# Optimization experiments

Measured on AMD Instinct MI355X. Metric: run time of the kernel, lower is better.

The kernel has to match this reference:

```python
import jax, jax.numpy as jnp
import numpy as np

H, B, I = 1024, 64, 128
W_SCALE = 0.192
BETA = 10.0 / W_SCALE   # softplus-like sharpness 'b' in source
DT = 0.1
DELTA_T = 1.0
Z_MIN, Z_MAX = 0.001, 0.1


def setup_inputs() -> dict:
    key = jax.random.key(0)
    ks = jax.random.split(key, 12)
    s = 1.0 / np.sqrt(H)  # nn.init.uniform_(param, -1/sqrt(H), 1/sqrt(H))
    u = lambda k, shp: jax.random.uniform(k, shp, jnp.float32, -s, s)
    return {
        "x": jax.random.normal(ks[0], (I, B), jnp.float32),
        "v_t": jnp.zeros((B, H), jnp.float32),
        "X": jnp.ones((B, H, H), jnp.float32),            # depression state x=1
        "U": jnp.full((B, H, H), 0.9, jnp.float32),       # facilitation state U=0.9
        "raw_w_r": u(ks[1], (H, H)),
        "p_r": u(ks[2], (H, I)),
        "b_r": u(ks[3], (H, 1)),
        "g_z": u(ks[4], (H, 1)),
        "c_x": u(ks[5], (H, H)),
        "c_u": u(ks[6], (H, H)),
        "c_U": u(ks[7], (H, H)),
        "a_exc": jax.random.uniform(ks[8], (), jnp.float32, -s, s),
        "a_inh": jax.random.uniform(ks[9], (), jnp.float32, -s, s),
    }


def reference(x, v_t, X, U, raw_w_r, p_r, b_r, g_z, c_x, c_u, c_U, a_exc, a_inh):
    sig = jax.nn.sigmoid
    # rectified recurrent weights: (1/b) * log(cosh(b * raw)) -- same formula in
    # all four quadrants of the source, so apply it to the whole matrix.
    w_r = jnp.log(jnp.cosh(BETA * raw_w_r)) / BETA          # (H, H), >= 0
    w_z = jnp.abs(w_r)
    p_z = jnp.abs(p_r)
    # Dale gain: excitatory gain for first half of rows, inhibitory for second.
    a = jnp.concatenate([jnp.full((H // 2, 1), 1.0) * a_exc,
                         jnp.full((H // 2, 1), 1.0) * a_inh], axis=0)
    A = 10.0 * sig(a)                                        # (H, 1)

    vt = v_t.T                                               # (H, B)
    r = sig(vt)                                              # (H, B) firing rates
    rb = r.T[:, :, None]                                     # (B, H, 1) -> r_t[j,b]

    # synaptic depression X: X' = z_x + (1-z_x)X - dt * U * X * r_pre
    z_x = Z_MIN + (Z_MAX - Z_MIN) * sig(c_x)                 # (H, H)
    X_new = z_x + (1.0 - z_x) * X - DELTA_T * U * (X * rb)   # (B, H, H)

    # synaptic facilitation U: U' = Ucap*z_u + (1-z_u)U + dt * Ucap * (1-U) * r_pre
    z_u = Z_MIN + (Z_MAX - Z_MIN) * sig(c_u)
    Ucap = 0.9 * sig(c_U)                                    # (H, H)
    U_new = Ucap * z_u + (1.0 - z_u) * U + DELTA_T * Ucap * ((1.0 - U) * rb)
    U_new = jnp.clip(U_new, jax.lax.stop_gradient(Ucap)[None], 1.0)

    # gate z_t = dt * sigmoid(w_z (A*r) + p_z x + g_z)
    z_t = DT * sig(w_z @ (A * r) + p_z @ x + g_z)            # (H, B)

    # membrane update: per-batch effective weights (X*U*w_r) applied to rates
    rec = jnp.einsum('bjk,kb->jb', X_new * U_new * w_r, r)   # (H, B)
    v_new = (1.0 - z_t) * vt + DT * (rec + p_r @ x + b_r)    # (H, B)
    v_new = v_new.T                                          # (B, H)

    return v_new
```

## Files before the change

### kernel.cpp

```cpp
#include <hip/hip_runtime.h>
#include <cstddef>

#define Hdim 1024
#define Bdim 64
#define Idim 128

#define BETA_F 52.083333333333336f
#define INV_BETA_F 0.0192f
#define LN2_F 0.6931471805599453f

__device__ __forceinline__ float sigf(float x) {
    return 1.0f / (1.0f + __expf(-x));
}

__device__ __forceinline__ float logcoshf_(float t) {
    float a = fabsf(t);
    return a + log1pf(__expf(-2.0f * a)) - LN2_F;
}

__global__ void pre_kernel(const float* __restrict__ x,
                           const float* __restrict__ v_t,
                           const float* __restrict__ p_r,
                           const float* __restrict__ b_r,
                           const float* __restrict__ g_z,
                           float* __restrict__ r_ws,
                           float* __restrict__ membx,
                           float* __restrict__ gatex) {
    const int j = blockIdx.x;
    const int b = threadIdx.x;
    const float* pr = p_r + (size_t)j * Idim;
    float accm = 0.0f, accg = 0.0f;
#pragma unroll 4
    for (int i = 0; i < Idim; ++i) {
        float p  = pr[i];
        float xv = x[i * Bdim + b];
        accm = fmaf(p, xv, accm);
        accg = fmaf(fabsf(p), xv, accg);
    }
    membx[j * Bdim + b] = accm + b_r[j];
    gatex[j * Bdim + b] = accg + g_z[j];

    int id = j * Bdim + b;
    r_ws[id] = sigf(v_t[id]);
}

__global__ __launch_bounds__(256, 4) void main_kernel(
    const float* __restrict__ X,
    const float* __restrict__ U,
    const float* __restrict__ raw_w_r,
    const float* __restrict__ c_x,
    const float* __restrict__ c_u,
    const float* __restrict__ c_U,
    const float* __restrict__ v_t,
    const float* __restrict__ a_exc,
    const float* __restrict__ a_inh,
    const float* __restrict__ r_ws,
    const float* __restrict__ membx,
    const float* __restrict__ gatex,
    float* __restrict__ out) {
    __shared__ __align__(16) float s_zx[Hdim];
    __shared__ __align__(16) float s_zu[Hdim];
    __shared__ __align__(16) float s_uc[Hdim];
    __shared__ __align__(16) float s_wr[Hdim];
    __shared__ __align__(16) float s_wa[Hdim];

    const int j   = blockIdx.x;
    const int tid = threadIdx.x;

    const float Aexc = 10.0f * sigf(a_exc[0]);
    const float Ainh = 10.0f * sigf(a_inh[0]);

    {
        const int k = tid * 4;
        const size_t ro = (size_t)j * Hdim + k;
        float4 rw = *(const float4*)(raw_w_r + ro);
        float4 cx = *(const float4*)(c_x + ro);
        float4 cu = *(const float4*)(c_u + ro);
        float4 cN = *(const float4*)(c_U + ro);
        const float A = (k < Hdim / 2) ? Aexc : Ainh;

        float w0 = logcoshf_(BETA_F * rw.x) * INV_BETA_F;
        float w1 = logcoshf_(BETA_F * rw.y) * INV_BETA_F;
        float w2 = logcoshf_(BETA_F * rw.z) * INV_BETA_F;
        float w3 = logcoshf_(BETA_F * rw.w) * INV_BETA_F;
        s_wr[k + 0] = w0; s_wa[k + 0] = w0 * A;
        s_wr[k + 1] = w1; s_wa[k + 1] = w1 * A;
        s_wr[k + 2] = w2; s_wa[k + 2] = w2 * A;
        s_wr[k + 3] = w3; s_wa[k + 3] = w3 * A;

        s_zx[k + 0] = 0.001f + 0.099f * sigf(cx.x);
        s_zx[k + 1] = 0.001f + 0.099f * sigf(cx.y);
        s_zx[k + 2] = 0.001f + 0.099f * sigf(cx.z);
        s_zx[k + 3] = 0.001f + 0.099f * sigf(cx.w);

        s_zu[k + 0] = 0.001f + 0.099f * sigf(cu.x);
        s_zu[k + 1] = 0.001f + 0.099f * sigf(cu.y);
        s_zu[k + 2] = 0.001f + 0.099f * sigf(cu.z);
        s_zu[k + 3] = 0.001f + 0.099f * sigf(cu.w);

        s_uc[k + 0] = 0.9f * sigf(cN.x);
        s_uc[k + 1] = 0.9f * sigf(cN.y);
        s_uc[k + 2] = 0.9f * sigf(cN.z);
        s_uc[k + 3] = 0.9f * sigf(cN.w);
    }
    __syncthreads();

    const int wave = tid >> 6;
    const int lane = tid & 63;

    for (int b = wave; b < Bdim; b += 4) {
        const float* Xb = X + (size_t)b * Hdim * Hdim + (size_t)j * Hdim;
        const float* Ub = U + (size_t)b * Hdim * Hdim + (size_t)j * Hdim;
        const float* rb = r_ws + b * Hdim;
        const float rj = rb[j];

        float rec = 0.0f, gate = 0.0f;
#pragma unroll
        for (int it = 0; it < 4; ++it) {
            const int k = (it * 64 + lane) * 4;
            float4 Xv = *(const float4*)(Xb + k);
            float4 Uv = *(const float4*)(Ub + k);
            float4 rv = *(const float4*)(rb + k);
            float4 zx = *(const float4*)(s_zx + k);
            float4 zu = *(const float4*)(s_zu + k);
            float4 uc = *(const float4*)(s_uc + k);
            float4 wr = *(const float4*)(s_wr + k);
            float4 wa = *(const float4*)(s_wa + k);

#define COMPONENT(c)                                                          \
    {                                                                         \
        float xn = zx.c + (1.0f - zx.c) * Xv.c - Uv.c * Xv.c * rj;            \
        float un = uc.c * zu.c + (1.0f - zu.c) * Uv.c +                       \
                   uc.c * (1.0f - Uv.c) * rj;                                 \
        un = fminf(fmaxf(un, uc.c), 1.0f);                                    \
        rec  = fmaf(xn * un * wr.c, rv.c, rec);                               \
        gate = fmaf(wa.c, rv.c, gate);                                        \
    }
            COMPONENT(x)
            COMPONENT(y)
            COMPONENT(z)
            COMPONENT(w)
#undef COMPONENT
        }

#pragma unroll
        for (int off = 32; off > 0; off >>= 1) {
            rec  += __shfl_xor(rec, off, 64);
            gate += __shfl_xor(gate, off, 64);
        }

        if (lane == 0) {
            float z  = 0.1f * sigf(gate + gatex[j * Bdim + b]);
            float vt = v_t[(size_t)b * Hdim + j];
            float vn = (1.0f - z) * vt + 0.1f * (rec + membx[j * Bdim + b]);
            out[(size_t)b * Hdim + j] = vn;
        }
    }
}

extern "C" void kernel_launch(void* const* d_in, const int* in_sizes, int n_in,
                              void* d_out, int out_size, void* d_ws, size_t ws_size,
                              hipStream_t stream) {
    const float* x       = (const float*)d_in[0];
    const float* v_t     = (const float*)d_in[1];
    const float* X       = (const float*)d_in[2];
    const float* U       = (const float*)d_in[3];
    const float* raw_w_r = (const float*)d_in[4];
    const float* p_r     = (const float*)d_in[5];
    const float* b_r     = (const float*)d_in[6];
    const float* g_z     = (const float*)d_in[7];
    const float* c_x     = (const float*)d_in[8];
    const float* c_u     = (const float*)d_in[9];
    const float* c_U     = (const float*)d_in[10];
    const float* a_exc   = (const float*)d_in[11];
    const float* a_inh   = (const float*)d_in[12];

    float* out = (float*)d_out;

    float* r_ws  = (float*)d_ws;
    float* membx = r_ws + Bdim * Hdim;
    float* gatex = membx + Hdim * Bdim;

    pre_kernel<<<dim3(Hdim), dim3(Bdim), 0, stream>>>(
        x, v_t, p_r, b_r, g_z, r_ws, membx, gatex);

    main_kernel<<<dim3(Hdim), dim3(256), 0, stream>>>(
        X, U, raw_w_r, c_x, c_u, c_U, v_t, a_exc, a_inh,
        r_ws, membx, gatex, out);
}
```

Before: 550.8 us.

## Split batch across grid y and batch 4 rows per wave for memory parallelism

The main kernel grid becomes 1024x4, with each wave handling 4 batch entries at once. Loads for X, U and r are issued for all 4 entries before the arithmetic, which raises memory-level parallelism on the bandwidth-bound stream over the 2x256MB X/U tensors. The A-weighted shared array is dropped; the gate is accumulated as separate excitatory and inhibitory partial sums and scaled by A at the end. In exchange, each of the 4 blocks per row recomputes the per-row logcosh and sigmoid tables, and register pressure rises.

```diff
diff --git a/kernel.cpp b/kernel.cpp
--- a/kernel.cpp
+++ b/kernel.cpp
@@ -62,13 +62,9 @@
     __shared__ __align__(16) float s_zu[Hdim];
     __shared__ __align__(16) float s_uc[Hdim];
     __shared__ __align__(16) float s_wr[Hdim];
-    __shared__ __align__(16) float s_wa[Hdim];
 
     const int j   = blockIdx.x;
     const int tid = threadIdx.x;
-
-    const float Aexc = 10.0f * sigf(a_exc[0]);
-    const float Ainh = 10.0f * sigf(a_inh[0]);
 
     {
         const int k = tid * 4;
@@ -77,16 +73,11 @@
         float4 cx = *(const float4*)(c_x + ro);
         float4 cu = *(const float4*)(c_u + ro);
         float4 cN = *(const float4*)(c_U + ro);
-        const float A = (k < Hdim / 2) ? Aexc : Ainh;
-
-        float w0 = logcoshf_(BETA_F * rw.x) * INV_BETA_F;
-        float w1 = logcoshf_(BETA_F * rw.y) * INV_BETA_F;
-        float w2 = logcoshf_(BETA_F * rw.z) * INV_BETA_F;
-        float w3 = logcoshf_(BETA_F * rw.w) * INV_BETA_F;
-        s_wr[k + 0] = w0; s_wa[k + 0] = w0 * A;
-        s_wr[k + 1] = w1; s_wa[k + 1] = w1 * A;
-        s_wr[k + 2] = w2; s_wa[k + 2] = w2 * A;
-        s_wr[k + 3] = w3; s_wa[k + 3] = w3 * A;
+
+        s_wr[k + 0] = logcoshf_(BETA_F * rw.x) * INV_BETA_F;
+        s_wr[k + 1] = logcoshf_(BETA_F * rw.y) * INV_BETA_F;
+        s_wr[k + 2] = logcoshf_(BETA_F * rw.z) * INV_BETA_F;
+        s_wr[k + 3] = logcoshf_(BETA_F * rw.w) * INV_BETA_F;
 
         s_zx[k + 0] = 0.001f + 0.099f * sigf(cx.x);
         s_zx[k + 1] = 0.001f + 0.099f * sigf(cx.y);
@@ -107,52 +98,85 @@
 
     const int wave = tid >> 6;
     const int lane = tid & 63;
-
-    for (int b = wave; b < Bdim; b += 4) {
-        const float* Xb = X + (size_t)b * Hdim * Hdim + (size_t)j * Hdim;
-        const float* Ub = U + (size_t)b * Hdim * Hdim + (size_t)j * Hdim;
-        const float* rb = r_ws + b * Hdim;
-        const float rj = rb[j];
-
-        float rec = 0.0f, gate = 0.0f;
-#pragma unroll
-        for (int it = 0; it < 4; ++it) {
-            const int k = (it * 64 + lane) * 4;
-            float4 Xv = *(const float4*)(Xb + k);
-            float4 Uv = *(const float4*)(Ub + k);
-            float4 rv = *(const float4*)(rb + k);
-            float4 zx = *(const float4*)(s_zx + k);
-            float4 zu = *(const float4*)(s_zu + k);
-            float4 uc = *(const float4*)(s_uc + k);
-            float4 wr = *(const float4*)(s_wr + k);
-            float4 wa = *(const float4*)(s_wa + k);
-
+    const int b0   = blockIdx.y * 16 + wave * 4;
+
+    const float* Xr[4];
+    const float* Ur[4];
+    const float* rr[4];
+    float rj[4];
+#pragma unroll
+    for (int bb = 0; bb < 4; ++bb) {
+        const int b = b0 + bb;
+        Xr[bb] = X + ((size_t)b * Hdim + j) * Hdim;
+        Ur[bb] = U + ((size_t)b * Hdim + j) * Hdim;
+        rr[bb] = r_ws + b * Hdim;
+        rj[bb] = rr[bb][j];
+    }
+
+    float rec[4] = {0.f, 0.f, 0.f, 0.f};
+    float ge[4]  = {0.f, 0.f, 0.f, 0.f};
+    float gi[4]  = {0.f, 0.f, 0.f, 0.f};
+
+#pragma unroll
+    for (int chunk = 0; chunk < 4; ++chunk) {
+        const int k = (chunk * 64 + lane) * 4;
+        float4 zx = *(const float4*)(s_zx + k);
+        float4 zu = *(const float4*)(s_zu + k);
+        float4 uc = *(const float4*)(s_uc + k);
+        float4 wr = *(const float4*)(s_wr + k);
+
+        float4 Xv[4], Uv[4], rv[4];
+#pragma unroll
+        for (int bb = 0; bb < 4; ++bb) {
+            Xv[bb] = *(const float4*)(Xr[bb] + k);
+            Uv[bb] = *(const float4*)(Ur[bb] + k);
+            rv[bb] = *(const float4*)(rr[bb] + k);
+        }
+
+#pragma unroll
+        for (int bb = 0; bb < 4; ++bb) {
+            float g = 0.0f;
 #define COMPONENT(c)                                                          \
     {                                                                         \
-        float xn = zx.c + (1.0f - zx.c) * Xv.c - Uv.c * Xv.c * rj;            \
-        float un = uc.c * zu.c + (1.0f - zu.c) * Uv.c +                       \
-                   uc.c * (1.0f - Uv.c) * rj;                                 \
+        float xn = zx.c + (1.0f - zx.c) * Xv[bb].c - Uv[bb].c * Xv[bb].c * rj[bb]; \
+        float un = uc.c * zu.c + (1.0f - zu.c) * Uv[bb].c +                   \
+                   uc.c * (1.0f - Uv[bb].c) * rj[bb];                         \
         un = fminf(fmaxf(un, uc.c), 1.0f);                                    \
-        rec  = fmaf(xn * un * wr.c, rv.c, rec);                               \
-        gate = fmaf(wa.c, rv.c, gate);                                        \
+        rec[bb] = fmaf(xn * un * wr.c, rv[bb].c, rec[bb]);                    \
+        g       = fmaf(wr.c, rv[bb].c, g);                                    \
     }
             COMPONENT(x)
             COMPONENT(y)
             COMPONENT(z)
             COMPONENT(w)
 #undef COMPONENT
-        }
-
-#pragma unroll
-        for (int off = 32; off > 0; off >>= 1) {
-            rec  += __shfl_xor(rec, off, 64);
-            gate += __shfl_xor(gate, off, 64);
-        }
-
-        if (lane == 0) {
-            float z  = 0.1f * sigf(gate + gatex[j * Bdim + b]);
+            if (chunk < 2) ge[bb] += g; else gi[bb] += g;
+        }
+    }
+
+    const float Aexc = 10.0f * sigf(a_exc[0]);
+    const float Ainh = 10.0f * sigf(a_inh[0]);
+    float gate[4];
+#pragma unroll
+    for (int bb = 0; bb < 4; ++bb)
+        gate[bb] = fmaf(Aexc, ge[bb], Ainh * gi[bb]);
+
+#pragma unroll
+    for (int off = 32; off > 0; off >>= 1) {
+#pragma unroll
+        for (int bb = 0; bb < 4; ++bb) {
+            rec[bb]  += __shfl_xor(rec[bb], off, 64);
+            gate[bb] += __shfl_xor(gate[bb], off, 64);
+        }
+    }
+
+    if (lane == 0) {
+#pragma unroll
+        for (int bb = 0; bb < 4; ++bb) {
+            const int b = b0 + bb;
+            float z  = 0.1f * sigf(gate[bb] + gatex[j * Bdim + b]);
             float vt = v_t[(size_t)b * Hdim + j];
-            float vn = (1.0f - z) * vt + 0.1f * (rec + membx[j * Bdim + b]);
+            float vn = (1.0f - z) * vt + 0.1f * (rec[bb] + membx[j * Bdim + b]);
             out[(size_t)b * Hdim + j] = vn;
         }
     }
@@ -184,7 +208,7 @@
     pre_kernel<<<dim3(Hdim), dim3(Bdim), 0, stream>>>(
         x, v_t, p_r, b_r, g_z, r_ws, membx, gatex);
 
-    main_kernel<<<dim3(Hdim), dim3(256), 0, stream>>>(
+    main_kernel<<<dim3(Hdim, 4), dim3(256), 0, stream>>>(
         X, U, raw_w_r, c_x, c_u, c_U, v_t, a_exc, a_inh,
         r_ws, membx, gatex, out);
 }
```

Result: slower. 568.7 us (+3.2%).

## Precompute transformed weights and process two batches per wave

Applied to the files above, without the earlier changes.

Moves the logcosh and sigmoid transforms of the H×H parameter matrices into a separate elementwise kernel whose outputs go to workspace. The main kernel now gives each wave one row j and two batch entries, reusing the loaded parameter vectors across both batches. The gate computation applies the Dale gain after the reduction instead of storing a scaled copy of the weights. This adds a kernel launch and extra workspace traffic for four H×H arrays, and keeps a fallback path that recomputes the transforms inline when the workspace is too small. The dominant cost is still streaming the large X and U tensors.

```diff
diff --git a/kernel.cpp b/kernel.cpp
--- a/kernel.cpp
+++ b/kernel.cpp
@@ -44,13 +44,51 @@
     r_ws[id] = sigf(v_t[id]);
 }
 
-__global__ __launch_bounds__(256, 4) void main_kernel(
-    const float* __restrict__ X,
-    const float* __restrict__ U,
+__global__ __launch_bounds__(256) void transform_kernel(
     const float* __restrict__ raw_w_r,
     const float* __restrict__ c_x,
     const float* __restrict__ c_u,
     const float* __restrict__ c_U,
+    float* __restrict__ t_wr,
+    float* __restrict__ t_zx,
+    float* __restrict__ t_zu,
+    float* __restrict__ t_uc) {
+    const int i = (blockIdx.x * 256 + threadIdx.x) * 4;
+    float4 rw = *(const float4*)(raw_w_r + i);
+    float4 cx = *(const float4*)(c_x + i);
+    float4 cu = *(const float4*)(c_u + i);
+    float4 cN = *(const float4*)(c_U + i);
+    float4 o;
+    o.x = logcoshf_(BETA_F * rw.x) * INV_BETA_F;
+    o.y = logcoshf_(BETA_F * rw.y) * INV_BETA_F;
+    o.z = logcoshf_(BETA_F * rw.z) * INV_BETA_F;
+    o.w = logcoshf_(BETA_F * rw.w) * INV_BETA_F;
+    *(float4*)(t_wr + i) = o;
+    o.x = 0.001f + 0.099f * sigf(cx.x);
+    o.y = 0.001f + 0.099f * sigf(cx.y);
+    o.z = 0.001f + 0.099f * sigf(cx.z);
+    o.w = 0.001f + 0.099f * sigf(cx.w);
+    *(float4*)(t_zx + i) = o;
+    o.x = 0.001f + 0.099f * sigf(cu.x);
+    o.y = 0.001f + 0.099f * sigf(cu.y);
+    o.z = 0.001f + 0.099f * sigf(cu.z);
+    o.w = 0.001f + 0.099f * sigf(cu.w);
+    *(float4*)(t_zu + i) = o;
+    o.x = 0.9f * sigf(cN.x);
+    o.y = 0.9f * sigf(cN.y);
+    o.z = 0.9f * sigf(cN.z);
+    o.w = 0.9f * sigf(cN.w);
+    *(float4*)(t_uc + i) = o;
+}
+
+template <bool PRECOMP>
+__global__ __launch_bounds__(256, 8) void main_kernel(
+    const float* __restrict__ X,
+    const float* __restrict__ U,
+    const float* __restrict__ pw_,
+    const float* __restrict__ pzx_,
+    const float* __restrict__ pzu_,
+    const float* __restrict__ puc_,
     const float* __restrict__ v_t,
     const float* __restrict__ a_exc,
     const float* __restrict__ a_inh,
@@ -58,102 +96,120 @@
     const float* __restrict__ membx,
     const float* __restrict__ gatex,
     float* __restrict__ out) {
-    __shared__ __align__(16) float s_zx[Hdim];
-    __shared__ __align__(16) float s_zu[Hdim];
-    __shared__ __align__(16) float s_uc[Hdim];
-    __shared__ __align__(16) float s_wr[Hdim];
-    __shared__ __align__(16) float s_wa[Hdim];
-
-    const int j   = blockIdx.x;
-    const int tid = threadIdx.x;
+    const int wave = threadIdx.x >> 6;
+    const int lane = threadIdx.x & 63;
+    const int j    = blockIdx.y * 4 + wave;
+    const int b0   = blockIdx.x * 2;
+
+    const size_t prow = (size_t)j * Hdim;
+    const float* pw  = pw_  + prow;
+    const float* pzx = pzx_ + prow;
+    const float* pzu = pzu_ + prow;
+    const float* puc = puc_ + prow;
+
+    const float* X0 = X + ((size_t)b0 * Hdim + j) * Hdim;
+    const float* X1 = X0 + (size_t)Hdim * Hdim;
+    const float* U0 = U + ((size_t)b0 * Hdim + j) * Hdim;
+    const float* U1 = U0 + (size_t)Hdim * Hdim;
+    const float* rr0 = r_ws + b0 * Hdim;
+    const float* rr1 = rr0 + Hdim;
+
+    const float rj0 = rr0[j];
+    const float rj1 = rr1[j];
+
+    float rec0 = 0.f, rec1 = 0.f;
+    float ge0 = 0.f, ge1 = 0.f;
+    float gi0 = 0.f, gi1 = 0.f;
+
+#pragma unroll
+    for (int chunk = 0; chunk < 4; ++chunk) {
+        const int k = (chunk * 64 + lane) * 4;
+        float4 wr, zx, zu, uc;
+        if (PRECOMP) {
+            wr = *(const float4*)(pw + k);
+            zx = *(const float4*)(pzx + k);
+            zu = *(const float4*)(pzu + k);
+            uc = *(const float4*)(puc + k);
+        } else {
+            float4 rw = *(const float4*)(pw + k);
+            float4 cx = *(const float4*)(pzx + k);
+            float4 cu = *(const float4*)(pzu + k);
+            float4 cN = *(const float4*)(puc + k);
+            wr.x = logcoshf_(BETA_F * rw.x) * INV_BETA_F;
+            wr.y = logcoshf_(BETA_F * rw.y) * INV_BETA_F;
+            wr.z = logcoshf_(BETA_F * rw.z) * INV_BETA_F;
+            wr.w = logcoshf_(BETA_F * rw.w) * INV_BETA_F;
+            zx.x = 0.001f + 0.099f * sigf(cx.x);
+            zx.y = 0.001f + 0.099f * sigf(cx.y);
+            zx.z = 0.001f + 0.099f * sigf(cx.z);
+            zx.w = 0.001f + 0.099f * sigf(cx.w);
+            zu.x = 0.001f + 0.099f * sigf(cu.x);
+            zu.y = 0.001f + 0.099f * sigf(cu.y);
+            zu.z = 0.001f + 0.099f * sigf(cu.z);
+            zu.w = 0.001f + 0.099f * sigf(cu.w);
+            uc.x = 0.9f * sigf(cN.x);
+            uc.y = 0.9f * sigf(cN.y);
+            uc.z = 0.9f * sigf(cN.z);
+            uc.w = 0.9f * sigf(cN.w);
+        }
+        float4 r0 = *(const float4*)(rr0 + k);
+        float4 r1 = *(const float4*)(rr1 + k);
+        float4 Xv0 = *(const float4*)(X0 + k);
+        float4 Uv0 = *(const float4*)(U0 + k);
+        float4 Xv1 = *(const float4*)(X1 + k);
+        float4 Uv1 = *(const float4*)(U1 + k);
+
+        float g0 = 0.f, g1 = 0.f;
+#define COMPONENT(c)                                                          \
+    {                                                                         \
+        float xn0 = zx.c + (1.0f - zx.c) * Xv0.c - Uv0.c * Xv0.c * rj0;       \
+        float un0 = uc.c * zu.c + (1.0f - zu.c) * Uv0.c +                     \
+                    uc.c * (1.0f - Uv0.c) * rj0;                              \
+        un0 = fminf(fmaxf(un0, uc.c), 1.0f);                                  \
+        rec0 = fmaf(xn0 * un0 * wr.c, r0.c, rec0);                            \
+        g0   = fmaf(wr.c, r0.c, g0);                                          \
+        float xn1 = zx.c + (1.0f - zx.c) * Xv1.c - Uv1.c * Xv1.c * rj1;       \
+        float un1 = uc.c * zu.c + (1.0f - zu.c) * Uv1.c +                     \
+                    uc.c * (1.0f - Uv1.c) * rj1;                              \
+        un1 = fminf(fmaxf(un1, uc.c), 1.0f);                                  \
+        rec1 = fmaf(xn1 * un1 * wr.c, r1.c, rec1);                            \
+        g1   = fmaf(wr.c, r1.c, g1);                                          \
+    }
+        COMPONENT(x)
+        COMPONENT(y)
+        COMPONENT(z)
+        COMPONENT(w)
+#undef COMPONENT
+        if (chunk < 2) { ge0 += g0; ge1 += g1; }
+        else           { gi0 += g0; gi1 += g1; }
+    }
 
     const float Aexc = 10.0f * sigf(a_exc[0]);
     const float Ainh = 10.0f * sigf(a_inh[0]);
-
-    {
-        const int k = tid * 4;
-        const size_t ro = (size_t)j * Hdim + k;
-        float4 rw = *(const float4*)(raw_w_r + ro);
-        float4 cx = *(const float4*)(c_x + ro);
-        float4 cu = *(const float4*)(c_u + ro);
-        float4 cN = *(const float4*)(c_U + ro);
-        const float A = (k < Hdim / 2) ? Aexc : Ainh;
-
-        float w0 = logcoshf_(BETA_F * rw.x) * INV_BETA_F;
-        float w1 = logcoshf_(BETA_F * rw.y) * INV_BETA_F;
-        float w2 = logcoshf_(BETA_F * rw.z) * INV_BETA_F;
-        float w3 = logcoshf_(BETA_F * rw.w) * INV_BETA_F;
-        s_wr[k + 0] = w0; s_wa[k + 0] = w0 * A;
-        s_wr[k + 1] = w1; s_wa[k + 1] = w1 * A;
-        s_wr[k + 2] = w2; s_wa[k + 2] = w2 * A;
-        s_wr[k + 3] = w3; s_wa[k + 3] = w3 * A;
-
-        s_zx[k + 0] = 0.001f + 0.099f * sigf(cx.x);
-        s_zx[k + 1] = 0.001f + 0.099f * sigf(cx.y);
-        s_zx[k + 2] = 0.001f + 0.099f * sigf(cx.z);
-        s_zx[k + 3] = 0.001f + 0.099f * sigf(cx.w);
-
-        s_zu[k + 0] = 0.001f + 0.099f * sigf(cu.x);
-        s_zu[k + 1] = 0.001f + 0.099f * sigf(cu.y);
-        s_zu[k + 2] = 0.001f + 0.099f * sigf(cu.z);
-        s_zu[k + 3] = 0.001f + 0.099f * sigf(cu.w);
-
-        s_uc[k + 0] = 0.9f * sigf(cN.x);
-        s_uc[k + 1] = 0.9f * sigf(cN.y);
-        s_uc[k + 2] = 0.9f * sigf(cN.z);
-        s_uc[k + 3] = 0.9f * sigf(cN.w);
-    }
-    __syncthreads();
-
-    const int wave = tid >> 6;
-    const int lane = tid & 63;
-
-    for (int b = wave; b < Bdim; b += 4) {
-        const float* Xb = X + (size_t)b * Hdim * Hdim + (size_t)j * Hdim;
-        const float* Ub = U + (size_t)b * Hdim * Hdim + (size_t)j * Hdim;
-        const float* rb = r_ws + b * Hdim;
-        const float rj = rb[j];
-
-        float rec = 0.0f, gate = 0.0f;
+    float gate0 = fmaf(Aexc, ge0, Ainh * gi0);
+    float gate1 = fmaf(Aexc, ge1, Ainh * gi1);
+
 #pragma unroll
-        for (int it = 0; it < 4; ++it) {
-            const int k = (it * 64 + lane) * 4;
-            float4 Xv = *(const float4*)(Xb + k);
-            float4 Uv = *(const float4*)(Ub + k);
-            float4 rv = *(const float4*)(rb + k);
-            float4 zx = *(const float4*)(s_zx + k);
-            float4 zu = *(const float4*)(s_zu + k);
-            float4 uc = *(const float4*)(s_uc + k);
-            float4 wr = *(const float4*)(s_wr + k);
-            float4 wa = *(const float4*)(s_wa + k);
-
-#define COMPONENT(c)                                                          \
-    {                                                                         \
-        float xn = zx.c + (1.0f - zx.c) * Xv.c - Uv.c * Xv.c * rj;            \
-        float un = uc.c * zu.c + (1.0f - zu.c) * Uv.c +                       \
-                   uc.c * (1.0f - Uv.c) * rj;                                 \
-        un = fminf(fmaxf(un, uc.c), 1.0f);                                    \
-        rec  = fmaf(xn * un * wr.c, rv.c, rec);                               \
-        gate = fmaf(wa.c, rv.c, gate);                                        \
-    }
-            COMPONENT(x)
-            COMPONENT(y)
-            COMPONENT(z)
-            COMPONENT(w)
-#undef COMPONENT
+    for (int off = 32; off > 0; off >>= 1) {
+        rec0  += __shfl_xor(rec0, off, 64);
+        rec1  += __shfl_xor(rec1, off, 64);
+        gate0 += __shfl_xor(gate0, off, 64);
+        gate1 += __shfl_xor(gate1, off, 64);
+    }
+
+    if (lane == 0) {
+        {
+            float z  = 0.1f * sigf(gate0 + gatex[j * Bdim + b0]);
+            float vt = v_t[(size_t)b0 * Hdim + j];
+            out[(size_t)b0 * Hdim + j] =
+                (1.0f - z) * vt + 0.1f * (rec0 + membx[j * Bdim + b0]);
         }
-
-#pragma unroll
-        for (int off = 32; off > 0; off >>= 1) {
-            rec  += __shfl_xor(rec, off, 64);
-            gate += __shfl_xor(gate, off, 64);
-        }
-
-        if (lane == 0) {
-            float z  = 0.1f * sigf(gate + gatex[j * Bdim + b]);
+        {
+            const int b = b0 + 1;
+            float z  = 0.1f * sigf(gate1 + gatex[j * Bdim + b]);
             float vt = v_t[(size_t)b * Hdim + j];
-            float vn = (1.0f - z) * vt + 0.1f * (rec + membx[j * Bdim + b]);
-            out[(size_t)b * Hdim + j] = vn;
+            out[(size_t)b * Hdim + j] =
+                (1.0f - z) * vt + 0.1f * (rec1 + membx[j * Bdim + b]);
         }
     }
 }
@@ -180,11 +236,26 @@
     float* r_ws  = (float*)d_ws;
     float* membx = r_ws + Bdim * Hdim;
     float* gatex = membx + Hdim * Bdim;
+    float* t_wr  = gatex + Hdim * Bdim;
+    float* t_zx  = t_wr + (size_t)Hdim * Hdim;
+    float* t_zu  = t_zx + (size_t)Hdim * Hdim;
+    float* t_uc  = t_zu + (size_t)Hdim * Hdim;
+
+    const size_t needed =
+        (size_t)(3 * Bdim * Hdim + 4 * Hdim * Hdim) * sizeof(float);
 
     pre_kernel<<<dim3(Hdim), dim3(Bdim), 0, stream>>>(
         x, v_t, p_r, b_r, g_z, r_ws, membx, gatex);
 
-    main_kernel<<<dim3(Hdim), dim3(256), 0, stream>>>(
-        X, U, raw_w_r, c_x, c_u, c_U, v_t, a_exc, a_inh,
-        r_ws, membx, gatex, out);
-}
+    if (ws_size >= needed) {
+        transform_kernel<<<dim3(Hdim * Hdim / (256 * 4)), dim3(256), 0, stream>>>(
+            raw_w_r, c_x, c_u, c_U, t_wr, t_zx, t_zu, t_uc);
+        main_kernel<true><<<dim3(Bdim / 2, Hdim / 4), dim3(256), 0, stream>>>(
+            X, U, t_wr, t_zx, t_zu, t_uc, v_t, a_exc, a_inh,
+            r_ws, membx, gatex, out);
+    } else {
+        main_kernel<false><<<dim3(Bdim / 2, Hdim / 4), dim3(256), 0, stream>>>(
+            X, U, raw_w_r, c_x, c_u, c_U, v_t, a_exc, a_inh,
+            r_ws, membx, gatex, out);
+    }
+}
```

New measurement: 596.7 us. +8.3%, slower.

## Split batch across 2D grid and hoist all X/U loads for two batches

Applied to the files above, without the earlier changes.

The main kernel grid becomes (H, 2), so each block handles 32 batches and each wave handles 8, processed two at a time. All sixteen float4 X/U loads for the batch pair are issued up front to raise memory-level parallelism. The shared s_wa array is dropped and the Dale gain is applied after accumulating separate excitatory and inhibitory partial sums. The cost is doubled per-block prologue work (logcosh and sigmoid tables recomputed by twice as many blocks) and higher register pressure.

```diff
diff --git a/kernel.cpp b/kernel.cpp
--- a/kernel.cpp
+++ b/kernel.cpp
@@ -62,13 +62,9 @@
     __shared__ __align__(16) float s_zu[Hdim];
     __shared__ __align__(16) float s_uc[Hdim];
     __shared__ __align__(16) float s_wr[Hdim];
-    __shared__ __align__(16) float s_wa[Hdim];
 
     const int j   = blockIdx.x;
     const int tid = threadIdx.x;
-
-    const float Aexc = 10.0f * sigf(a_exc[0]);
-    const float Ainh = 10.0f * sigf(a_inh[0]);
 
     {
         const int k = tid * 4;
@@ -77,16 +73,11 @@
         float4 cx = *(const float4*)(c_x + ro);
         float4 cu = *(const float4*)(c_u + ro);
         float4 cN = *(const float4*)(c_U + ro);
-        const float A = (k < Hdim / 2) ? Aexc : Ainh;
-
-        float w0 = logcoshf_(BETA_F * rw.x) * INV_BETA_F;
-        float w1 = logcoshf_(BETA_F * rw.y) * INV_BETA_F;
-        float w2 = logcoshf_(BETA_F * rw.z) * INV_BETA_F;
-        float w3 = logcoshf_(BETA_F * rw.w) * INV_BETA_F;
-        s_wr[k + 0] = w0; s_wa[k + 0] = w0 * A;
-        s_wr[k + 1] = w1; s_wa[k + 1] = w1 * A;
-        s_wr[k + 2] = w2; s_wa[k + 2] = w2 * A;
-        s_wr[k + 3] = w3; s_wa[k + 3] = w3 * A;
+
+        s_wr[k + 0] = logcoshf_(BETA_F * rw.x) * INV_BETA_F;
+        s_wr[k + 1] = logcoshf_(BETA_F * rw.y) * INV_BETA_F;
+        s_wr[k + 2] = logcoshf_(BETA_F * rw.z) * INV_BETA_F;
+        s_wr[k + 3] = logcoshf_(BETA_F * rw.w) * INV_BETA_F;
 
         s_zx[k + 0] = 0.001f + 0.099f * sigf(cx.x);
         s_zx[k + 1] = 0.001f + 0.099f * sigf(cx.y);
@@ -107,53 +98,114 @@
 
     const int wave = tid >> 6;
     const int lane = tid & 63;
-
-    for (int b = wave; b < Bdim; b += 4) {
-        const float* Xb = X + (size_t)b * Hdim * Hdim + (size_t)j * Hdim;
-        const float* Ub = U + (size_t)b * Hdim * Hdim + (size_t)j * Hdim;
-        const float* rb = r_ws + b * Hdim;
-        const float rj = rb[j];
-
-        float rec = 0.0f, gate = 0.0f;
-#pragma unroll
-        for (int it = 0; it < 4; ++it) {
-            const int k = (it * 64 + lane) * 4;
-            float4 Xv = *(const float4*)(Xb + k);
-            float4 Uv = *(const float4*)(Ub + k);
-            float4 rv = *(const float4*)(rb + k);
-            float4 zx = *(const float4*)(s_zx + k);
-            float4 zu = *(const float4*)(s_zu + k);
-            float4 uc = *(const float4*)(s_uc + k);
-            float4 wr = *(const float4*)(s_wr + k);
-            float4 wa = *(const float4*)(s_wa + k);
-
-#define COMPONENT(c)                                                          \
+    const int base = blockIdx.y * 32 + wave * 8;
+
+    const float Aexc = 10.0f * sigf(a_exc[0]);
+    const float Ainh = 10.0f * sigf(a_inh[0]);
+
+    for (int it = 0; it < 4; ++it) {
+        const int b0 = base + 2 * it;
+        const float* X0 = X + ((size_t)b0 * Hdim + j) * Hdim;
+        const float* X1 = X0 + (size_t)Hdim * Hdim;
+        const float* U0 = U + ((size_t)b0 * Hdim + j) * Hdim;
+        const float* U1 = U0 + (size_t)Hdim * Hdim;
+        const float* rr0 = r_ws + b0 * Hdim;
+        const float* rr1 = rr0 + Hdim;
+
+        float4 xa0, xa1, xa2, xa3, ua0, ua1, ua2, ua3;
+        float4 xb0, xb1, xb2, xb3, ub0, ub1, ub2, ub3;
+        {
+            const int k0 = lane * 4;
+            xa0 = *(const float4*)(X0 + k0 + 0);
+            xa1 = *(const float4*)(X0 + k0 + 256);
+            xa2 = *(const float4*)(X0 + k0 + 512);
+            xa3 = *(const float4*)(X0 + k0 + 768);
+            ua0 = *(const float4*)(U0 + k0 + 0);
+            ua1 = *(const float4*)(U0 + k0 + 256);
+            ua2 = *(const float4*)(U0 + k0 + 512);
+            ua3 = *(const float4*)(U0 + k0 + 768);
+            xb0 = *(const float4*)(X1 + k0 + 0);
+            xb1 = *(const float4*)(X1 + k0 + 256);
+            xb2 = *(const float4*)(X1 + k0 + 512);
+            xb3 = *(const float4*)(X1 + k0 + 768);
+            ub0 = *(const float4*)(U1 + k0 + 0);
+            ub1 = *(const float4*)(U1 + k0 + 256);
+            ub2 = *(const float4*)(U1 + k0 + 512);
+            ub3 = *(const float4*)(U1 + k0 + 768);
+        }
+
+        const float rj0 = rr0[j];
+        const float rj1 = rr1[j];
+
+        float rec0 = 0.f, rec1 = 0.f;
+        float ge0 = 0.f, ge1 = 0.f;
+        float gi0 = 0.f, gi1 = 0.f;
+
+#define CHUNK(c, Xa, Ua, Xb, Ub, GA0, GA1)                                    \
     {                                                                         \
-        float xn = zx.c + (1.0f - zx.c) * Xv.c - Uv.c * Xv.c * rj;            \
-        float un = uc.c * zu.c + (1.0f - zu.c) * Uv.c +                       \
-                   uc.c * (1.0f - Uv.c) * rj;                                 \
-        un = fminf(fmaxf(un, uc.c), 1.0f);                                    \
-        rec  = fmaf(xn * un * wr.c, rv.c, rec);                               \
-        gate = fmaf(wa.c, rv.c, gate);                                        \
-    }
-            COMPONENT(x)
-            COMPONENT(y)
-            COMPONENT(z)
-            COMPONENT(w)
+        const int k = c * 256 + lane * 4;                                     \
+        float4 zx = *(const float4*)(s_zx + k);                               \
+        float4 zu = *(const float4*)(s_zu + k);                               \
+        float4 uc = *(const float4*)(s_uc + k);                               \
+        float4 wr = *(const float4*)(s_wr + k);                               \
+        float4 r0v = *(const float4*)(rr0 + k);                               \
+        float4 r1v = *(const float4*)(rr1 + k);                               \
+        float g0 = 0.f, g1 = 0.f;                                             \
+        COMPONENT(x, Xa, Ua, Xb, Ub)                                          \
+        COMPONENT(y, Xa, Ua, Xb, Ub)                                          \
+        COMPONENT(z, Xa, Ua, Xb, Ub)                                          \
+        COMPONENT(w, Xa, Ua, Xb, Ub)                                          \
+        GA0 += g0;                                                            \
+        GA1 += g1;                                                            \
+    }
+#define COMPONENT(c, Xa, Ua, Xb, Ub)                                          \
+    {                                                                         \
+        float xn0 = zx.c + (1.0f - zx.c) * Xa.c - Ua.c * Xa.c * rj0;          \
+        float un0 = uc.c * zu.c + (1.0f - zu.c) * Ua.c +                      \
+                    uc.c * (1.0f - Ua.c) * rj0;                               \
+        un0 = fminf(fmaxf(un0, uc.c), 1.0f);                                  \
+        rec0 = fmaf(xn0 * un0 * wr.c, r0v.c, rec0);                           \
+        g0   = fmaf(wr.c, r0v.c, g0);                                         \
+        float xn1 = zx.c + (1.0f - zx.c) * Xb.c - Ub.c * Xb.c * rj1;          \
+        float un1 = uc.c * zu.c + (1.0f - zu.c) * Ub.c +                      \
+                    uc.c * (1.0f - Ub.c) * rj1;                               \
+        un1 = fminf(fmaxf(un1, uc.c), 1.0f);                                  \
+        rec1 = fmaf(xn1 * un1 * wr.c, r1v.c, rec1);                           \
+        g1   = fmaf(wr.c, r1v.c, g1);                                         \
+    }
+
+        CHUNK(0, xa0, ua0, xb0, ub0, ge0, ge1)
+        CHUNK(1, xa1, ua1, xb1, ub1, ge0, ge1)
+        CHUNK(2, xa2, ua2, xb2, ub2, gi0, gi1)
+        CHUNK(3, xa3, ua3, xb3, ub3, gi0, gi1)
 #undef COMPONENT
-        }
+#undef CHUNK
+
+        float gate0 = fmaf(Aexc, ge0, Ainh * gi0);
+        float gate1 = fmaf(Aexc, ge1, Ainh * gi1);
 
 #pragma unroll
         for (int off = 32; off > 0; off >>= 1) {
-            rec  += __shfl_xor(rec, off, 64);
-            gate += __shfl_xor(gate, off, 64);
+            rec0  += __shfl_xor(rec0, off, 64);
+            rec1  += __shfl_xor(rec1, off, 64);
+            gate0 += __shfl_xor(gate0, off, 64);
+            gate1 += __shfl_xor(gate1, off, 64);
         }
 
         if (lane == 0) {
-            float z  = 0.1f * sigf(gate + gatex[j * Bdim + b]);
-            float vt = v_t[(size_t)b * Hdim + j];
-            float vn = (1.0f - z) * vt + 0.1f * (rec + membx[j * Bdim + b]);
-            out[(size_t)b * Hdim + j] = vn;
+            {
+                float z  = 0.1f * sigf(gate0 + gatex[j * Bdim + b0]);
+                float vt = v_t[(size_t)b0 * Hdim + j];
+                out[(size_t)b0 * Hdim + j] =
+                    (1.0f - z) * vt + 0.1f * (rec0 + membx[j * Bdim + b0]);
+            }
+            {
+                const int b = b0 + 1;
+                float z  = 0.1f * sigf(gate1 + gatex[j * Bdim + b]);
+                float vt = v_t[(size_t)b * Hdim + j];
+                out[(size_t)b * Hdim + j] =
+                    (1.0f - z) * vt + 0.1f * (rec1 + membx[j * Bdim + b]);
+            }
         }
     }
 }
@@ -184,7 +236,7 @@
     pre_kernel<<<dim3(Hdim), dim3(Bdim), 0, stream>>>(
         x, v_t, p_r, b_r, g_z, r_ws, membx, gatex);
 
-    main_kernel<<<dim3(Hdim), dim3(256), 0, stream>>>(
+    main_kernel<<<dim3(Hdim, 2), dim3(256), 0, stream>>>(
         X, U, raw_w_r, c_x, c_u, c_U, v_t, a_exc, a_inh,
         r_ws, membx, gatex, out);
 }
```

Measured after the change: 594.5 us. 1.08x slower.
